# Optimization experiments

Measured on AMD Instinct MI355X. Metric: run time of the kernel, lower is better.

The kernel has to match this reference:

```python
import jax, jax.numpy as jnp
import numpy as np

N_NODES = 50000
N_EDGES = 800000
NUM_FEATURES = 128
HIDDEN = 128
NUM_CLASSES = 10
NUM_GRAPHS = 512
PROCESSING_STEPS = 4


def setup_inputs() -> dict:
    key = jax.random.key(0)
    ks = jax.random.split(key, 20)
    s = 0.05
    inp = {
        'x': jax.random.normal(ks[0], (N_NODES, NUM_FEATURES), jnp.float32),
        'edge_index': jax.random.randint(ks[1], (2, N_EDGES), 0, N_NODES),
        'batch': jnp.sort(jax.random.randint(ks[2], (N_NODES,), 0, NUM_GRAPHS)),
        # GCN layers (weights stored [in, out])
        'W1': jax.random.normal(ks[3], (NUM_FEATURES, HIDDEN), jnp.float32) * s,
        'b1': jnp.zeros((HIDDEN,), jnp.float32),
        'W2': jax.random.normal(ks[4], (HIDDEN, HIDDEN), jnp.float32) * s,
        'b2': jnp.zeros((HIDDEN,), jnp.float32),
        'W3': jax.random.normal(ks[5], (HIDDEN, HIDDEN), jnp.float32) * s,
        'b3': jnp.zeros((HIDDEN,), jnp.float32),
        # Set2Set LSTM cell: input 2*HIDDEN -> hidden HIDDEN, torch gate order i,f,g,o
        'Wih': jax.random.normal(ks[6], (4 * HIDDEN, 2 * HIDDEN), jnp.float32) * s,
        'Whh': jax.random.normal(ks[7], (4 * HIDDEN, HIDDEN), jnp.float32) * s,
        'bih': jnp.zeros((4 * HIDDEN,), jnp.float32),
        'bhh': jnp.zeros((4 * HIDDEN,), jnp.float32),
        # MLP head
        'L1w': jax.random.normal(ks[8], (2 * HIDDEN, HIDDEN), jnp.float32) * s,
        'L1b': jnp.zeros((HIDDEN,), jnp.float32),
        'L2w': jax.random.normal(ks[9], (HIDDEN, HIDDEN // 2), jnp.float32) * s,
        'L2b': jnp.zeros((HIDDEN // 2,), jnp.float32),
        'L3w': jax.random.normal(ks[10], (HIDDEN // 2, NUM_CLASSES), jnp.float32) * s,
        'L3b': jnp.zeros((NUM_CLASSES,), jnp.float32),
    }
    return inp


def _gcn_conv(x, row, col, W, b, n):
    # PyG GCNConv: x @ W, symmetric normalization with self-loops, scatter-add to targets.
    xw = x @ W  # [N, out]
    deg = jax.ops.segment_sum(jnp.ones_like(col, dtype=xw.dtype), col, num_segments=n)
    dis = jnp.where(deg > 0, jax.lax.rsqrt(jnp.maximum(deg, 1.0)), 0.0)
    norm = dis[row] * dis[col]  # [E+N]
    out = jax.ops.segment_sum(norm[:, None] * xw[row], col, num_segments=n)
    return out + b


def _segment_softmax(e, batch, n_seg):
    emax = jax.lax.stop_gradient(jax.ops.segment_max(e, batch, num_segments=n_seg))
    emax = jnp.where(jnp.isfinite(emax), emax, 0.0)
    a = jnp.exp(e - emax[batch])
    asum = jax.ops.segment_sum(a, batch, num_segments=n_seg)
    return a / jnp.where(asum > 0, asum, 1.0)[batch]


def reference(x, edge_index, batch, W1, b1, W2, b2, W3, b3,
              Wih, Whh, bih, bhh, L1w, L1b, L2w, L2b, L3w, L3b):
    n = x.shape[0]
    # add self loops once
    loops = jnp.arange(n, dtype=edge_index.dtype)
    row = jnp.concatenate([edge_index[0], loops])  # sources
    col = jnp.concatenate([edge_index[1], loops])  # targets

    h = jax.nn.relu(_gcn_conv(x, row, col, W1, b1, n))
    h = jax.nn.relu(_gcn_conv(h, row, col, W2, b2, n))
    h = jax.nn.relu(_gcn_conv(h, row, col, W3, b3, n))

    # Set2Set readout (processing_steps=4)
    d = h.shape[1]
    hs = jnp.zeros((NUM_GRAPHS, d), h.dtype)
    cs = jnp.zeros((NUM_GRAPHS, d), h.dtype)
    q_star = jnp.zeros((NUM_GRAPHS, 2 * d), h.dtype)
    for _ in range(PROCESSING_STEPS):
        gates = q_star @ Wih.T + hs @ Whh.T + bih + bhh  # [B, 4d]
        ig, fg, gg, og = jnp.split(gates, 4, axis=-1)
        cs = jax.nn.sigmoid(fg) * cs + jax.nn.sigmoid(ig) * jnp.tanh(gg)
        q = jax.nn.sigmoid(og) * jnp.tanh(cs)
        hs = q
        e = jnp.sum(h * q[batch], axis=-1)  # [N]
        a = _segment_softmax(e, batch, NUM_GRAPHS)
        r = jax.ops.segment_sum(a[:, None] * h, batch, num_segments=NUM_GRAPHS)
        q_star = jnp.concatenate([q, r], axis=-1)

    # MLP head (dropout inactive in eval)
    y = jax.nn.relu(q_star @ L1w + L1b)
    y = jax.nn.relu(y @ L2w + L2b)
    y = y @ L3w + L3b
    return jax.nn.log_softmax(y, axis=-1)
```

## Files before the change

### kernel.cpp

```cpp
#include <hip/hip_runtime.h>

constexpr int NN  = 50000;
constexpr int NE  = 800000;
constexpr int FD  = 128;
constexpr int NG  = 512;
constexpr int CAP = 96;
constexpr int NBKT   = 196;
constexpr int BNODES = 256;
constexpr int CAPB   = 6144;

typedef __attribute__((ext_vector_type(8))) short bf16x8;
typedef __attribute__((ext_vector_type(4))) float f32x4;

__device__ __forceinline__ float bf2f(unsigned short u) {
    unsigned int v = ((unsigned int)u) << 16;
    float f; __builtin_memcpy(&f, &v, 4); return f;
}
__device__ __forceinline__ unsigned short f2bf(float f) {
    unsigned int u; __builtin_memcpy(&u, &f, 4);
    u += 0x7FFFu + ((u >> 16) & 1u);
    return (unsigned short)(u >> 16);
}
__device__ __forceinline__ float2 bfp(unsigned int u) {
    unsigned int lo = u << 16, hi = u & 0xFFFF0000u;
    float2 r; __builtin_memcpy(&r.x, &lo, 4); __builtin_memcpy(&r.y, &hi, 4);
    return r;
}
__device__ __forceinline__ unsigned int packbf(float a, float b) {
    return (unsigned int)f2bf(a) | ((unsigned int)f2bf(b) << 16);
}
__device__ __forceinline__ float sigmoidf(float x) { return 1.0f / (1.0f + __expf(-x)); }
__device__ __forceinline__ float ldw(const void* p, int idx, int flag) {
    return flag ? ((const float*)p)[idx] : bf2f(((const unsigned short*)p)[idx]);
}

__global__ void k_detect(const unsigned int* __restrict__ xw, int* __restrict__ flag,
                         int* __restrict__ gcnt) {
    if (threadIdx.x < NBKT) gcnt[threadIdx.x] = 0;
    __shared__ int cnt;
    if (threadIdx.x == 0) cnt = 0;
    __syncthreads();
    int local = 0;
    for (int i = threadIdx.x; i < 2048; i += 256) {
        unsigned int w = xw[i];
        unsigned int h0 = w & 0xFFFFu, h1 = w >> 16;
        if (((h0 >> 7) & 0xFF) >= 0x90) local++;
        if (((h1 >> 7) & 0xFF) >= 0x90) local++;
    }
    atomicAdd(&cnt, local);
    __syncthreads();
    if (threadIdx.x == 0) *flag = (cnt > 256) ? 1 : 0;
}

__global__ void k_cvt_x(const void* __restrict__ src, unsigned short* __restrict__ dst,
                        const int* __restrict__ batch, int* __restrict__ goff,
                        const int* __restrict__ flagp) {
    int i = blockIdx.x * 256 + threadIdx.x;
    if (i < NN * FD / 8) {
        if (*flagp) {
            const float4* s = (const float4*)src;
            float4 a = s[2 * i], b = s[2 * i + 1];
            uint4 o;
            o.x = packbf(a.x, a.y); o.y = packbf(a.z, a.w);
            o.z = packbf(b.x, b.y); o.w = packbf(b.z, b.w);
            ((uint4*)dst)[i] = o;
        } else {
            ((uint4*)dst)[i] = ((const uint4*)src)[i];
        }
    }
    if (i < NN) {
        int b = batch[i];
        if (b < 0) b = 0;
        if (b >= NG) b = NG - 1;
        int prev;
        if (i == 0) prev = -1;
        else {
            prev = batch[i - 1];
            if (prev < 0) prev = 0;
            if (prev >= NG) prev = NG - 1;
        }
        for (int g = prev + 1; g <= b; g++) goff[g] = i;
        if (i == NN - 1)
            for (int g = b + 1; g <= NG; g++) goff[g] = NN;
    }
}

struct WDesc {
    const void* src[12];
    void* dst[12];
    int kind[12];
    int off[13];
};
__global__ void k_cvt_w(WDesc d, const int* __restrict__ flagp) {
    int gid = blockIdx.x * 256 + threadIdx.x;
    if (gid >= d.off[12]) return;
    int flag = *flagp;
    int t = 0;
    while (gid >= d.off[t + 1]) t++;
    int i = gid - d.off[t];
    if (d.kind[t] == 0) {
        if (flag) ((unsigned short*)d.dst[t])[i] = f2bf(((const float*)d.src[t])[i]);
        else      ((unsigned short*)d.dst[t])[i] = ((const unsigned short*)d.src[t])[i];
    } else {
        int n = i >> 6, k2 = i & 63;
        ((unsigned int*)d.dst[t])[i] = packbf(ldw(d.src[t], (2 * k2) * 128 + n, flag),
                                              ldw(d.src[t], (2 * k2 + 1) * 128 + n, flag));
    }
}

__global__ void k_wt(const void* __restrict__ Wih, const void* __restrict__ Whh,
                     const void* __restrict__ bih, const void* __restrict__ bhh,
                     unsigned int* __restrict__ WcombT,
                     unsigned int* __restrict__ WrT,
                     float* __restrict__ bsum, const int* __restrict__ flagp) {
    int gid = blockIdx.x * 256 + threadIdx.x;
    int flag = *flagp;
    if (gid < 64 * 512) {
        int k2 = gid >> 9, row = gid & 511;
        float a0 = ldw(Wih, row * 256 + 2 * k2, flag)     + ldw(Whh, row * 128 + 2 * k2, flag);
        float a1 = ldw(Wih, row * 256 + 2 * k2 + 1, flag) + ldw(Whh, row * 128 + 2 * k2 + 1, flag);
        WcombT[(k2 >> 1) * 1024 + 2 * row + (k2 & 1)] = packbf(a0, a1);
    } else if (gid < 2 * 64 * 512) {
        int g2 = gid - 64 * 512;
        int k2 = g2 >> 9, row = g2 & 511;
        WrT[(k2 >> 1) * 1024 + 2 * row + (k2 & 1)] =
            packbf(ldw(Wih, row * 256 + 128 + 2 * k2, flag),
                   ldw(Wih, row * 256 + 128 + 2 * k2 + 1, flag));
    } else if (gid < 2 * 64 * 512 + 512) {
        int row = gid - 2 * 64 * 512;
        bsum[row] = ldw(bih, row, flag) + ldw(bhh, row, flag);
    }
}

__global__ __launch_bounds__(256) void k_fill1(const int* __restrict__ ei,
                                               int* __restrict__ gcnt,
                                               unsigned int* __restrict__ bktbuf) {
    __shared__ int hist[NBKT];
    __shared__ int wbase[NBKT];
    int t = threadIdx.x;
    for (int i = t; i < NBKT; i += 256) hist[i] = 0;
    __syncthreads();
    int base_e = blockIdx.x * 2048;
    int bb[8], rk[8];
    unsigned int pk[8];
#pragma unroll
    for (int k = 0; k < 8; k++) {
        int e = base_e + k * 256 + t;
        if (e < NE) {
            int r = ei[e], c = ei[NE + e];
            if ((unsigned)r >= (unsigned)NN) r = 0;
            if ((unsigned)c >= (unsigned)NN) c = 0;
            bb[k] = c >> 8;
            rk[k] = atomicAdd(&hist[bb[k]], 1);
            pk[k] = ((unsigned)c << 16) | (unsigned)r;
        } else bb[k] = -1;
    }
    __syncthreads();
    for (int i = t; i < NBKT; i += 256)
        wbase[i] = hist[i] ? atomicAdd(&gcnt[i], hist[i]) : 0;
    __syncthreads();
#pragma unroll
    for (int k = 0; k < 8; k++) {
        if (bb[k] >= 0) {
            int pos = wbase[bb[k]] + rk[k];
            if (pos < CAPB) bktbuf[bb[k] * CAPB + pos] = pk[k];
        }
    }
}

__global__ __launch_bounds__(512) void k_fill2(const unsigned int* __restrict__ bktbuf,
                                               const int* __restrict__ gcnt,
                                               int* __restrict__ bcnt,
                                               unsigned short* __restrict__ csr_row) {
    int b = blockIdx.x, t = threadIdx.x;
    __shared__ int lcnt[BNODES];
    for (int i = t; i < BNODES; i += 512) lcnt[i] = 0;
    uint4* creg = (uint4*)(csr_row + (size_t)b * BNODES * CAP);
    for (int i = t; i < BNODES * CAP / 8; i += 512)
        creg[i] = (uint4){0, 0, 0, 0};
    __syncthreads();
    int n = gcnt[b]; if (n > CAPB) n = CAPB;
    const unsigned int* bp = bktbuf + (size_t)b * CAPB;
    for (int i = t; i < n; i += 512) {
        unsigned int v = bp[i];
        int r = v & 0xFFFFu;
        int c = v >> 16;
        int cl = c & (BNODES - 1);
        int pos = atomicAdd(&lcnt[cl], 1);
        if (pos < CAP)
            csr_row[(size_t)c * CAP + pos] = (unsigned short)r;
    }
    __syncthreads();
    for (int i = t; i < BNODES; i += 512) {
        int node = b * BNODES + i;
        if (node < NN) bcnt[node] = lcnt[i];
    }
}

__global__ __launch_bounds__(256) void k_gemm(const unsigned short* __restrict__ H,
                                              const unsigned int* __restrict__ WT,
                                              const int* __restrict__ counts,
                                              unsigned short* __restrict__ XW, int M) {
    __shared__ alignas(16) unsigned short WB[128 * 136];
    int t = threadIdx.x;
    unsigned int* WBu = (unsigned int*)WB;
    for (int c = t; c < 2048; c += 256) {
        uint4 v = ((const uint4*)WT)[c];
        int n = c >> 4, k2q = c & 15;
        *(uint4*)(WBu + n * 68 + k2q * 4) = v;
    }
    __syncthreads();
    int wave = t >> 6, lane = t & 63;
    int lm = lane & 15;
    int lq = lane >> 4;
    int row = blockIdx.x * 64 + wave * 16 + lm;
    int rowc = (row < M) ? row : (M - 1);
    const unsigned short* Arow = H + (size_t)rowc * 128;
    f32x4 acc[8];
#pragma unroll
    for (int n = 0; n < 8; n++) acc[n] = (f32x4){0.f, 0.f, 0.f, 0.f};
#pragma unroll
    for (int kk = 0; kk < 4; kk++) {
        bf16x8 afrag = *(const bf16x8*)(Arow + kk * 32 + lq * 8);
        const unsigned short* wbase = WB + kk * 32 + lq * 8;
#pragma unroll
        for (int n = 0; n < 8; n++) {
            bf16x8 bfrag = *(const bf16x8*)(wbase + (n * 16 + lm) * 136);
            acc[n] = __builtin_amdgcn_mfma_f32_16x16x32_bf16(afrag, bfrag, acc[n], 0, 0, 0);
        }
    }
    __syncthreads();
#pragma unroll
    for (int r = 0; r < 4; r++) {
        int row_local = wave * 16 + lq * 4 + r;
        int orow = blockIdx.x * 64 + row_local;
        int oc = (orow < M) ? orow : (M - 1);
        float dn = rsqrtf((float)(counts[oc] + 1));
#pragma unroll
        for (int n = 0; n < 8; n++)
            WB[row_local * 136 + n * 16 + lm] = f2bf(acc[n][r] * dn);
    }
#pragma unroll
    for (int it = 0; it < 4; it++) {
        int row_local = wave * 16 + it * 4 + (lane >> 4);
        int row_global = blockIdx.x * 64 + row_local;
        uint4 v = *(const uint4*)(WB + row_local * 136 + (lane & 15) * 8);
        if (row_global < M)
            *((uint4*)(XW + (size_t)row_global * 128) + (lane & 15)) = v;
    }
}

__global__ __launch_bounds__(256) void k_aggr(const unsigned short* __restrict__ XW,
                                              const int* __restrict__ counts,
                                              const unsigned short* __restrict__ csr_row,
                                              const unsigned short* __restrict__ bias,
                                              unsigned short* __restrict__ Hout) {
    int wave = threadIdx.x >> 6;
    int lane = threadIdx.x & 63;
    int nsel = lane >> 4;
    int sub  = lane & 15;
    int node = blockIdx.x * 16 + wave * 4 + nsel;
    if (node >= NN) return;
    const uint4* XW4 = (const uint4*)XW;
    int cnt = counts[node];
    float dn = rsqrtf((float)(cnt + 1));
    uint4 sv = XW4[(size_t)node * 16 + sub];
    float2 s0 = bfp(sv.x), s1 = bfp(sv.y), s2 = bfp(sv.z), s3 = bfp(sv.w);
    float a0 = s0.x, a1 = s0.y, a2 = s1.x, a3 = s1.y;
    float a4 = s2.x, a5 = s2.y, a6 = s3.x, a7 = s3.y;
    int n = (cnt < CAP) ? cnt : CAP;
    const unsigned short* lst = csr_row + (size_t)node * CAP;
    int j = 0;
    for (; j + 8 <= n; j += 8) {
        int r[8]; uint4 v[8];
#pragma unroll
        for (int k = 0; k < 8; k++) r[k] = lst[j + k];
#pragma unroll
        for (int k = 0; k < 8; k++) v[k] = XW4[(size_t)r[k] * 16 + sub];
#pragma unroll
        for (int k = 0; k < 8; k++) {
            float2 f;
            f = bfp(v[k].x); a0 += f.x; a1 += f.y;
            f = bfp(v[k].y); a2 += f.x; a3 += f.y;
            f = bfp(v[k].z); a4 += f.x; a5 += f.y;
            f = bfp(v[k].w); a6 += f.x; a7 += f.y;
        }
    }
    for (; j < n; j++) {
        int r = lst[j];
        uint4 v = XW4[(size_t)r * 16 + sub];
        float2 f;
        f = bfp(v.x); a0 += f.x; a1 += f.y;
        f = bfp(v.y); a2 += f.x; a3 += f.y;
        f = bfp(v.z); a4 += f.x; a5 += f.y;
        f = bfp(v.w); a6 += f.x; a7 += f.y;
    }
    uint4 bv = ((const uint4*)bias)[sub];
    float2 b0 = bfp(bv.x), b1 = bfp(bv.y), b2 = bfp(bv.z), b3 = bfp(bv.w);
    uint4 o;
    o.x = packbf(fmaxf(dn * a0 + b0.x, 0.0f), fmaxf(dn * a1 + b0.y, 0.0f));
    o.y = packbf(fmaxf(dn * a2 + b1.x, 0.0f), fmaxf(dn * a3 + b1.y, 0.0f));
    o.z = packbf(fmaxf(dn * a4 + b2.x, 0.0f), fmaxf(dn * a5 + b2.y, 0.0f));
    o.w = packbf(fmaxf(dn * a6 + b3.x, 0.0f), fmaxf(dn * a7 + b3.y, 0.0f));
    ((uint4*)Hout)[(size_t)node * 16 + sub] = o;
}

__global__ __launch_bounds__(512) void k_s2s(const unsigned short* __restrict__ H,
                                             const int* __restrict__ goff,
                                             const unsigned int* __restrict__ WcombT,
                                             const unsigned int* __restrict__ WrT,
                                             const float* __restrict__ bsum,
                                             const unsigned short* __restrict__ L1w,
                                             const unsigned short* __restrict__ L1b,
                                             const unsigned short* __restrict__ L2w,
                                             const unsigned short* __restrict__ L2b,
                                             const unsigned short* __restrict__ L3w,
                                             const unsigned short* __restrict__ L3b,
                                             void* __restrict__ out,
                                             const int* __restrict__ flagp) {
    int g = blockIdx.x, t = threadIdx.x;
    __shared__ float qsr[256];
    __shared__ float hsv[128], csv[128];
    __shared__ float gates[512];
    __shared__ float wred[8];
    __shared__ float wrr[8][128];
    __shared__ float ps[128];
    __shared__ float qrep[4 * 132];
    __shared__ float y1[128], y2[64], y3[10], lseS[1];

    if (t < 256) qsr[t] = 0.0f;
    if (t < 128) { hsv[t] = 0.0f; csv[t] = 0.0f; }
    __syncthreads();

    int s = goff[g], e = goff[g + 1];
    if (s < 0) s = 0;
    if (e > NN) e = NN;
    if (e < s) e = s;
    int w = t >> 6, lane = t & 63;
    const unsigned int* Hu = (const unsigned int*)H;

    int nq = t >> 2;
    int fq = (t & 3) * 16;
    const float* qc = qrep + (t & 3) * 132 + 2 * fq;
    const uint2* WC2 = (const uint2*)WcombT;
    const uint2* WR2 = (const uint2*)WrT;

    for (int step = 0; step < 4; step++) {
        {
            float accA = bsum[t], accB = 0.0f, accC = 0.0f, accD = 0.0f;
#pragma unroll 8
            for (int p = 0; p < 32; p++) {
                uint2 u = WC2[p * 512 + t];
                float2 w0 = bfp(u.x), w1 = bfp(u.y);
                accA += w0.x * hsv[4 * p];     accB += w0.y * hsv[4 * p + 1];
                accC += w1.x * hsv[4 * p + 2]; accD += w1.y * hsv[4 * p + 3];
            }
#pragma unroll 8
            for (int p = 0; p < 32; p++) {
                uint2 u = WR2[p * 512 + t];
                float2 w0 = bfp(u.x), w1 = bfp(u.y);
                accA += w0.x * qsr[128 + 4 * p];     accB += w0.y * qsr[128 + 4 * p + 1];
                accC += w1.x * qsr[128 + 4 * p + 2]; accD += w1.y * qsr[128 + 4 * p + 3];
            }
            gates[t] = (accA + accB) + (accC + accD);
        }
        __syncthreads();
        if (t < 128) {
            float ig = sigmoidf(gates[t]),       fg = sigmoidf(gates[128 + t]);
            float gg = tanhf(gates[256 + t]),    og = sigmoidf(gates[384 + t]);
            float c = fg * csv[t] + ig * gg;
            float q = og * tanhf(c);
            csv[t] = c;
            hsv[t] = q;
            qsr[t] = q;
            qrep[t] = q; qrep[132 + t] = q; qrep[264 + t] = q; qrep[396 + t] = q;
        }
        __syncthreads();

        float m = -1e30f, l = 0.0f, r0 = 0.0f, r1 = 0.0f;
        for (int cs = s; cs < e; cs += 128) {
            int ce = cs + 128; if (ce > e) ce = e;
            int nid = cs + nq;
            float eacc = 0.0f;
            if (nid < ce) {
                const unsigned int* hrow = Hu + (size_t)nid * 64 + fq;
#pragma unroll
                for (int u = 0; u < 16; u += 4) {
                    uint4 hv = *(const uint4*)(hrow + u);
                    float2 f0 = bfp(hv.x), f1 = bfp(hv.y);
                    float2 f2 = bfp(hv.z), f3 = bfp(hv.w);
                    const float* qp = qc + 2 * u;
                    eacc += f0.x * qp[0] + f0.y * qp[1] + f1.x * qp[2] + f1.y * qp[3]
                          + f2.x * qp[4] + f2.y * qp[5] + f3.x * qp[6] + f3.y * qp[7];
                }
            }
            eacc += __shfl_xor(eacc, 1);
            eacc += __shfl_xor(eacc, 2);
            float esc = (nid < ce) ? eacc : -1e30f;
            float vmax = esc;
            for (int d = 4; d < 64; d <<= 1) vmax = fmaxf(vmax, __shfl_xor(vmax, d));
            if (lane == 0) wred[w] = vmax;
            __syncthreads();
            float M = m;
#pragma unroll
            for (int k = 0; k < 8; k++) M = fmaxf(M, wred[k]);
            float p = __expf(esc - M);
            bool lead = ((t & 3) == 0) && (nid < ce);
            if (lead) ps[nq] = p;
            float psum = lead ? p : 0.0f;
            for (int d = 1; d < 64; d <<= 1) psum += __shfl_xor(psum, d);
            __syncthreads();
            if (lane == 0) wred[w] = psum;
            __syncthreads();
            float Lc = 0.0f;
#pragma unroll
            for (int k = 0; k < 8; k++) Lc += wred[k];
            float scale = __expf(m - M);
            l = l * scale + Lc;
            r0 *= scale; r1 *= scale;
            m = M;
            int i = cs + w;
            for (; i + 24 < ce; i += 32) {
                float p0 = ps[i - cs],      p1 = ps[i + 8 - cs];
                float p2 = ps[i + 16 - cs], p3 = ps[i + 24 - cs];
                unsigned int v0 = Hu[(size_t)i * 64 + lane];
                unsigned int v1 = Hu[(size_t)(i + 8) * 64 + lane];
                unsigned int v2 = Hu[(size_t)(i + 16) * 64 + lane];
                unsigned int v3 = Hu[(size_t)(i + 24) * 64 + lane];
                float2 f0 = bfp(v0), f1 = bfp(v1), f2 = bfp(v2), f3 = bfp(v3);
                r0 += p0 * f0.x + p1 * f1.x + p2 * f2.x + p3 * f3.x;
                r1 += p0 * f0.y + p1 * f1.y + p2 * f2.y + p3 * f3.y;
            }
            for (; i < ce; i += 8) {
                float p0 = ps[i - cs];
                float2 f = bfp(Hu[(size_t)i * 64 + lane]);
                r0 += p0 * f.x; r1 += p0 * f.y;
            }
            __syncthreads();
        }
        wrr[w][2 * lane]     = r0;
        wrr[w][2 * lane + 1] = r1;
        __syncthreads();
        if (t < 128) {
            float R = 0.0f;
#pragma unroll
            for (int k = 0; k < 8; k++) R += wrr[k][t];
            float L = l;
            if (!(L > 0.0f)) L = 1.0f;
            qsr[128 + t] = R / L;
        }
        __syncthreads();
    }

    if (t < 128) {
        float acc = bf2f(L1b[t]);
        for (int i = 0; i < 256; i++) acc += bf2f(L1w[i * 128 + t]) * qsr[i];
        y1[t] = fmaxf(acc, 0.0f);
    }
    __syncthreads();
    if (t < 64) {
        float a2 = bf2f(L2b[t]);
        for (int i = 0; i < 128; i++) a2 += bf2f(L2w[i * 64 + t]) * y1[i];
        y2[t] = fmaxf(a2, 0.0f);
    }
    __syncthreads();
    if (t < 10) {
        float a3 = bf2f(L3b[t]);
        for (int i = 0; i < 64; i++) a3 += bf2f(L3w[i * 10 + t]) * y2[i];
        y3[t] = a3;
    }
    __syncthreads();
    if (t == 0) {
        float m = y3[0];
        for (int i = 1; i < 10; i++) m = fmaxf(m, y3[i]);
        float s2 = 0.0f;
        for (int i = 0; i < 10; i++) s2 += __expf(y3[i] - m);
        lseS[0] = m + __logf(s2);
    }
    __syncthreads();
    if (t < 10) {
        float v = y3[t] - lseS[0];
        if (!(v == v)) v = -9.0f;
        if (*flagp) ((float*)out)[g * 10 + t] = v;
        else        ((unsigned short*)out)[g * 10 + t] = f2bf(v);
    }
}

extern "C" void kernel_launch(void* const* d_in, const int* in_sizes, int n_in,
                              void* d_out, int out_size, void* d_ws, size_t ws_size,
                              hipStream_t stream) {
    const int* ei  = (const int*)d_in[1];
    const int* bat = (const int*)d_in[2];

    char* base = (char*)d_ws;
    size_t woff = 0;
    auto alloc = [&](size_t bytes) -> void* {
        void* r = base + woff;
        woff = (woff + bytes + 255) & ~(size_t)255;
        return r;
    };
    unsigned short* A = (unsigned short*)alloc((size_t)NN * FD * 2);
    unsigned short* B = (unsigned short*)alloc((size_t)NN * FD * 2);
    unsigned short* csr_row = (unsigned short*)alloc((size_t)NBKT * BNODES * CAP * 2);
    int*   bcnt     = (int*)alloc((size_t)NN * 4);
    int*   goff     = (int*)alloc((NG + 1) * 4);
    int*   flag     = (int*)alloc(256);
    int*   gcnt     = (int*)alloc(NBKT * 4);
    unsigned int* WcombT = (unsigned int*)alloc(64 * 512 * 4);
    unsigned int* WrT    = (unsigned int*)alloc(64 * 512 * 4);
    float* bsum          = (float*)alloc(512 * 4);
    unsigned int* cWT1 = (unsigned int*)alloc(8192 * 4);
    unsigned int* cWT2 = (unsigned int*)alloc(8192 * 4);
    unsigned int* cWT3 = (unsigned int*)alloc(8192 * 4);
    auto walloc = [&](int n) { return (unsigned short*)alloc((size_t)n * 2); };
    unsigned short* cb1  = walloc(128);
    unsigned short* cb2  = walloc(128);
    unsigned short* cb3  = walloc(128);
    unsigned short* cL1w = walloc(256 * 128);
    unsigned short* cL1b = walloc(128);
    unsigned short* cL2w = walloc(128 * 64);
    unsigned short* cL2b = walloc(64);
    unsigned short* cL3w = walloc(64 * 10);
    unsigned short* cL3b = walloc(10);
    unsigned int* bktbuf = (unsigned int*)A;
    (void)ws_size; (void)in_sizes; (void)n_in; (void)out_size;

    k_detect<<<1, 256, 0, stream>>>((const unsigned int*)d_in[0], flag, gcnt);
    k_cvt_x<<<(NN * FD / 8 + 255) / 256, 256, 0, stream>>>(d_in[0], B, bat, goff, flag);
    {
        WDesc d;
        const int idxs[12]  = {3,    4,  5,    6,  7,    8,  13, 14, 15, 16, 17, 18};
        void* dsts[12]      = {cWT1, cb1, cWT2, cb2, cWT3, cb3,
                               cL1w, cL1b, cL2w, cL2b, cL3w, cL3b};
        const int kinds[12] = {1, 0, 1, 0, 1, 0, 0, 0, 0, 0, 0, 0};
        const int ns[12]    = {8192, 128, 8192, 128, 8192, 128,
                               256 * 128, 128, 128 * 64, 64, 64 * 10, 10};
        int acc = 0;
        for (int i = 0; i < 12; i++) {
            d.src[i] = d_in[idxs[i]];
            d.dst[i] = dsts[i];
            d.kind[i] = kinds[i];
            d.off[i] = acc;
            acc += ns[i];
        }
        d.off[12] = acc;
        k_cvt_w<<<(acc + 255) / 256, 256, 0, stream>>>(d, flag);
    }
    k_wt<<<(2 * 64 * 512 + 512 + 255) / 256, 256, 0, stream>>>(
        d_in[9], d_in[10], d_in[11], d_in[12], WcombT, WrT, bsum, flag);

    k_fill1<<<(NE + 2047) / 2048, 256, 0, stream>>>(ei, gcnt, bktbuf);
    k_fill2<<<NBKT, 512, 0, stream>>>(bktbuf, gcnt, bcnt, csr_row);

    const int gemmBlk = (NN + 63) / 64;
    const int aggrBlk = (NN + 15) / 16;

    k_gemm<<<gemmBlk, 256, 0, stream>>>(B, cWT1, bcnt, A, NN);
    k_aggr<<<aggrBlk, 256, 0, stream>>>(A, bcnt, csr_row, cb1, B);
    k_gemm<<<gemmBlk, 256, 0, stream>>>(B, cWT2, bcnt, A, NN);
    k_aggr<<<aggrBlk, 256, 0, stream>>>(A, bcnt, csr_row, cb2, B);
    k_gemm<<<gemmBlk, 256, 0, stream>>>(B, cWT3, bcnt, A, NN);
    k_aggr<<<aggrBlk, 256, 0, stream>>>(A, bcnt, csr_row, cb3, B);

    k_s2s<<<NG, 512, 0, stream>>>(B, goff, WcombT, WrT, bsum,
                                  cL1w, cL1b, cL2w, cL2b, cL3w, cL3b,
                                  d_out, flag);
}
```

Measured before the change: 327.8 us.

## Sort CSR neighbors by source slice, merge weight kernels, trim s2s barriers

k_fill2 now builds each node's neighbor list in two passes, grouping source indices into four row-range slices so that aggregation gathers walk memory with more locality. The weight conversion kernel is folded into k_wt to save one launch. Set2Set uses separate shared reduction slots for max and sum, which removes one barrier, and skips the trailing barrier on the last chunk. The extra counting pass in k_fill2 adds work and atomics in exchange.

```diff
diff --git a/kernel.cpp b/kernel.cpp
--- a/kernel.cpp
+++ b/kernel.cpp
@@ -4,7 +4,9 @@
 constexpr int NE  = 800000;
 constexpr int FD  = 128;
 constexpr int NG  = 512;
+constexpr int NB  = 4;
 constexpr int CAP = 96;
+constexpr int SLICE = 12500;
 constexpr int NBKT   = 196;
 constexpr int BNODES = 256;
 constexpr int CAPB   = 6144;
@@ -91,28 +93,12 @@
     int kind[12];
     int off[13];
 };
-__global__ void k_cvt_w(WDesc d, const int* __restrict__ flagp) {
-    int gid = blockIdx.x * 256 + threadIdx.x;
-    if (gid >= d.off[12]) return;
-    int flag = *flagp;
-    int t = 0;
-    while (gid >= d.off[t + 1]) t++;
-    int i = gid - d.off[t];
-    if (d.kind[t] == 0) {
-        if (flag) ((unsigned short*)d.dst[t])[i] = f2bf(((const float*)d.src[t])[i]);
-        else      ((unsigned short*)d.dst[t])[i] = ((const unsigned short*)d.src[t])[i];
-    } else {
-        int n = i >> 6, k2 = i & 63;
-        ((unsigned int*)d.dst[t])[i] = packbf(ldw(d.src[t], (2 * k2) * 128 + n, flag),
-                                              ldw(d.src[t], (2 * k2 + 1) * 128 + n, flag));
-    }
-}
-
 __global__ void k_wt(const void* __restrict__ Wih, const void* __restrict__ Whh,
                      const void* __restrict__ bih, const void* __restrict__ bhh,
                      unsigned int* __restrict__ WcombT,
                      unsigned int* __restrict__ WrT,
-                     float* __restrict__ bsum, const int* __restrict__ flagp) {
+                     float* __restrict__ bsum, WDesc d,
+                     const int* __restrict__ flagp) {
     int gid = blockIdx.x * 256 + threadIdx.x;
     int flag = *flagp;
     if (gid < 64 * 512) {
@@ -130,6 +116,19 @@
         int row = gid - 2 * 64 * 512;
         bsum[row] = ldw(bih, row, flag) + ldw(bhh, row, flag);
     }
+    if (gid < d.off[12]) {
+        int t = 0;
+        while (gid >= d.off[t + 1]) t++;
+        int i = gid - d.off[t];
+        if (d.kind[t] == 0) {
+            if (flag) ((unsigned short*)d.dst[t])[i] = f2bf(((const float*)d.src[t])[i]);
+            else      ((unsigned short*)d.dst[t])[i] = ((const unsigned short*)d.src[t])[i];
+        } else {
+            int n = i >> 6, k2 = i & 63;
+            ((unsigned int*)d.dst[t])[i] = packbf(ldw(d.src[t], (2 * k2) * 128 + n, flag),
+                                                  ldw(d.src[t], (2 * k2 + 1) * 128 + n, flag));
+        }
+    }
 }
 
 __global__ __launch_bounds__(256) void k_fill1(const int* __restrict__ ei,
@@ -173,8 +172,9 @@
                                                int* __restrict__ bcnt,
                                                unsigned short* __restrict__ csr_row) {
     int b = blockIdx.x, t = threadIdx.x;
-    __shared__ int lcnt[BNODES];
-    for (int i = t; i < BNODES; i += 512) lcnt[i] = 0;
+    __shared__ int lcnt[BNODES * NB];
+    __shared__ int loff[BNODES * NB];
+    for (int i = t; i < BNODES * NB; i += 512) lcnt[i] = 0;
     uint4* creg = (uint4*)(csr_row + (size_t)b * BNODES * CAP);
     for (int i = t; i < BNODES * CAP / 8; i += 512)
         creg[i] = (uint4){0, 0, 0, 0};
@@ -184,16 +184,33 @@
     for (int i = t; i < n; i += 512) {
         unsigned int v = bp[i];
         int r = v & 0xFFFFu;
+        int cl = (v >> 16) & (BNODES - 1);
+        int s = r / SLICE;
+        atomicAdd(&lcnt[cl * NB + s], 1);
+    }
+    __syncthreads();
+    if (t < BNODES) {
+        int c0 = lcnt[t * NB], c1 = lcnt[t * NB + 1];
+        int c2 = lcnt[t * NB + 2], c3 = lcnt[t * NB + 3];
+        loff[t * NB]     = 0;
+        loff[t * NB + 1] = c0;
+        loff[t * NB + 2] = c0 + c1;
+        loff[t * NB + 3] = c0 + c1 + c2;
+        int node = b * BNODES + t;
+        if (node < NN) bcnt[node] = c0 + c1 + c2 + c3;
+    }
+    __syncthreads();
+    for (int i = t; i < BNODES * NB; i += 512) lcnt[i] = 0;
+    __syncthreads();
+    for (int i = t; i < n; i += 512) {
+        unsigned int v = bp[i];
+        int r = v & 0xFFFFu;
         int c = v >> 16;
         int cl = c & (BNODES - 1);
-        int pos = atomicAdd(&lcnt[cl], 1);
+        int s = r / SLICE;
+        int pos = loff[cl * NB + s] + atomicAdd(&lcnt[cl * NB + s], 1);
         if (pos < CAP)
             csr_row[(size_t)c * CAP + pos] = (unsigned short)r;
-    }
-    __syncthreads();
-    for (int i = t; i < BNODES; i += 512) {
-        int node = b * BNODES + i;
-        if (node < NN) bcnt[node] = lcnt[i];
     }
 }
 
@@ -322,7 +339,7 @@
     __shared__ float qsr[256];
     __shared__ float hsv[128], csv[128];
     __shared__ float gates[512];
-    __shared__ float wred[8];
+    __shared__ float wredM[8], wredS[8];
     __shared__ float wrr[8][128];
     __shared__ float ps[128];
     __shared__ float qrep[4 * 132];
@@ -399,22 +416,21 @@
             float esc = (nid < ce) ? eacc : -1e30f;
             float vmax = esc;
             for (int d = 4; d < 64; d <<= 1) vmax = fmaxf(vmax, __shfl_xor(vmax, d));
-            if (lane == 0) wred[w] = vmax;
+            if (lane == 0) wredM[w] = vmax;
             __syncthreads();
             float M = m;
 #pragma unroll
-            for (int k = 0; k < 8; k++) M = fmaxf(M, wred[k]);
+            for (int k = 0; k < 8; k++) M = fmaxf(M, wredM[k]);
             float p = __expf(esc - M);
             bool lead = ((t & 3) == 0) && (nid < ce);
             if (lead) ps[nq] = p;
             float psum = lead ? p : 0.0f;
             for (int d = 1; d < 64; d <<= 1) psum += __shfl_xor(psum, d);
-            __syncthreads();
-            if (lane == 0) wred[w] = psum;
+            if (lane == 0) wredS[w] = psum;
             __syncthreads();
             float Lc = 0.0f;
 #pragma unroll
-            for (int k = 0; k < 8; k++) Lc += wred[k];
+            for (int k = 0; k < 8; k++) Lc += wredS[k];
             float scale = __expf(m - M);
             l = l * scale + Lc;
             r0 *= scale; r1 *= scale;
@@ -436,7 +452,7 @@
                 float2 f = bfp(Hu[(size_t)i * 64 + lane]);
                 r0 += p0 * f.x; r1 += p0 * f.y;
             }
-            __syncthreads();
+            if (ce < e) __syncthreads();
         }
         wrr[w][2 * lane]     = r0;
         wrr[w][2 * lane + 1] = r1;
@@ -544,10 +560,10 @@
             acc += ns[i];
         }
         d.off[12] = acc;
-        k_cvt_w<<<(acc + 255) / 256, 256, 0, stream>>>(d, flag);
-    }
-    k_wt<<<(2 * 64 * 512 + 512 + 255) / 256, 256, 0, stream>>>(
-        d_in[9], d_in[10], d_in[11], d_in[12], WcombT, WrT, bsum, flag);
+        int work = (2 * 64 * 512 + 512 > acc) ? (2 * 64 * 512 + 512) : acc;
+        k_wt<<<(work + 255) / 256, 256, 0, stream>>>(
+            d_in[9], d_in[10], d_in[11], d_in[12], WcombT, WrT, bsum, d, flag);
+    }
 
     k_fill1<<<(NE + 2047) / 2048, 256, 0, stream>>>(ei, gcnt, bktbuf);
     k_fill2<<<NBKT, 512, 0, stream>>>(bktbuf, gcnt, bcnt, csr_row);
```

Result: no change. 325.1 us (-0.8%).
